# Optimization experiments

Measured on AMD Instinct MI355X. Metric: run time of the kernel, lower is better.

The kernel has to match this reference:

```python
import jax, jax.numpy as jnp
import numpy as np

IN_F, HID, OUT = 128, 128, 32
N_NODES, N_EDGES, N_GRAPHS = 100000, 1600000, 64


def gcn_conv(x, W, b, src, dst, n):
    """PyG-style GCNConv: add self-loops, symmetric deg^-1/2 norm, linear, scatter-add."""
    h = x @ W  # [N, F_out]
    loop = jnp.arange(n)
    src_f = jnp.concatenate([src, loop])
    dst_f = jnp.concatenate([dst, loop])
    deg = jax.ops.segment_sum(jnp.ones_like(dst_f, dtype=x.dtype), dst_f, num_segments=n)
    dinv = jax.lax.rsqrt(jnp.maximum(deg, 1.0))  # deg >= 1 because of self-loops
    norm = dinv[src_f] * dinv[dst_f]             # [E+N]
    msg = h[src_f] * norm[:, None]               # gather + scale, [E+N, F_out]
    out = jax.ops.segment_sum(msg, dst_f, num_segments=n)  # scatter-add
    return out + b


def setup_inputs() -> dict:
    key = jax.random.key(0)
    ks = jax.random.split(key, 10)
    x = jax.random.normal(ks[0], (N_NODES, IN_F), dtype=jnp.float32)
    edge_index = jax.random.randint(ks[1], (2, N_EDGES), 0, N_NODES, dtype=jnp.int64)
    batch = jnp.sort(jax.random.randint(ks[2], (N_NODES,), 0, N_GRAPHS, dtype=jnp.int64))

    def glorot(k, fi, fo):
        s = np.sqrt(6.0 / (fi + fo)).astype(np.float32)
        return jax.random.uniform(k, (fi, fo), dtype=jnp.float32, minval=-s, maxval=s)

    return {
        "x": x,
        "edge_index": edge_index,
        "batch": batch,
        "num_graphs": N_GRAPHS,
        "W1": glorot(ks[3], IN_F, HID), "b1": jnp.zeros((HID,), jnp.float32),
        "W2": glorot(ks[4], HID, HID), "b2": jnp.zeros((HID,), jnp.float32),
        "W3": glorot(ks[5], HID, OUT), "b3": jnp.zeros((OUT,), jnp.float32),
    }


def reference(x, edge_index, batch, num_graphs, W1, b1, W2, b2, W3, b3):
    n = x.shape[0]
    src, dst = edge_index[0], edge_index[1]
    # Dropout is identity in eval mode.
    h = jax.nn.relu(gcn_conv(x, W1, b1, src, dst, n))
    h = jax.nn.relu(gcn_conv(h, W2, b2, src, dst, n))
    h = gcn_conv(h, W3, b3, src, dst, n)  # [N, OUT]
    # global_mean_pool over batch ids
    sums = jax.ops.segment_sum(h, batch, num_segments=num_graphs)
    cnts = jax.ops.segment_sum(jnp.ones((n,), h.dtype), batch, num_segments=num_graphs)
    x_global = sums / jnp.maximum(cnts, 1.0)[:, None]
    return h, x_global
```

## Files before the change

kernel.cpp:

```cpp
#include <hip/hip_runtime.h>
#include <hip/hip_bf16.h>


typedef unsigned int uint32;
typedef short short8 __attribute__((ext_vector_type(8)));
typedef float f32x4 __attribute__((ext_vector_type(4)));

#define BSH 7
#define MAXB 1024
#define BCH 8192

static __device__ __forceinline__ unsigned short f2bf(float f) {
    uint32 u = __float_as_uint(f);
    return (unsigned short)((u + 0x7fffu + ((u >> 16) & 1u)) >> 16);
}
static __device__ __forceinline__ float bf2f_lo(uint32 u) {
    return __uint_as_float(u << 16);
}
static __device__ __forceinline__ float bf2f_hi(uint32 u) {
    return __uint_as_float(u & 0xffff0000u);
}

__global__ __launch_bounds__(256) void zcnt_k(int* bcnt) {
    bcnt[blockIdx.x * 256 + threadIdx.x] = 0;
}

__global__ __launch_bounds__(256) void bhist_k(const int* __restrict__ dst, int E,
                                               int* __restrict__ bcnt) {
    __shared__ int h[MAXB];
    for (int i = threadIdx.x; i < MAXB; i += 256) h[i] = 0;
    __syncthreads();
    const int base = blockIdx.x * BCH;
    const int end = min(E, base + BCH);
    for (int e = base + (int)threadIdx.x; e < end; e += 256)
        atomicAdd(&h[__builtin_nontemporal_load(&dst[e]) >> BSH], 1);
    __syncthreads();
    for (int i = threadIdx.x; i < MAXB; i += 256)
        if (h[i]) atomicAdd(&bcnt[i], h[i]);
}

__global__ __launch_bounds__(256) void bscan_k(const int* __restrict__ bcnt,
                                               int* __restrict__ bstart,
                                               int* __restrict__ bcur, int B) {
    __shared__ int tot[256];
    const int tid = threadIdx.x;
    int v[4];
    int s = 0;
#pragma unroll
    for (int j = 0; j < 4; j++) {
        int idx = tid * 4 + j;
        v[j] = (idx < B) ? bcnt[idx] : 0;
        s += v[j];
    }
    tot[tid] = s;
    __syncthreads();
    for (int o = 1; o < 256; o <<= 1) {
        int t = (tid >= o) ? tot[tid - o] : 0;
        __syncthreads();
        tot[tid] += t;
        __syncthreads();
    }
    int run = tot[tid] - s;
#pragma unroll
    for (int j = 0; j < 4; j++) {
        int idx = tid * 4 + j;
        if (idx < B) {
            bstart[idx] = run;
            bcur[idx] = run;
            run += v[j];
        }
    }
    if (tid == 255) bstart[B] = run;
}

__global__ __launch_bounds__(256) void bfill_k(const int* __restrict__ src,
                                               const int* __restrict__ dst, int E,
                                               int* __restrict__ bcur,
                                               int* __restrict__ fifo) {
    __shared__ int h[MAXB];
    __shared__ int base[MAXB];
    for (int i = threadIdx.x; i < MAXB; i += 256) h[i] = 0;
    __syncthreads();
    const int b0 = blockIdx.x * BCH;
    const int end = min(E, b0 + BCH);
    for (int e = b0 + (int)threadIdx.x; e < end; e += 256)
        atomicAdd(&h[__builtin_nontemporal_load(&dst[e]) >> BSH], 1);
    __syncthreads();
    for (int i = threadIdx.x; i < MAXB; i += 256) {
        int c = h[i];
        base[i] = c ? atomicAdd(&bcur[i], c) : 0;
        h[i] = 0;
    }
    __syncthreads();
    for (int e = b0 + (int)threadIdx.x; e < end; e += 256) {
        int d = __builtin_nontemporal_load(&dst[e]);
        int s = __builtin_nontemporal_load(&src[e]);
        int b = d >> BSH;
        int off = base[b] + atomicAdd(&h[b], 1);
        fifo[off] = s | ((d & 127) << 20);
    }
}

__global__ __launch_bounds__(256) void bdeg_k(const int* __restrict__ fifo,
                                              const int* __restrict__ bstart,
                                              int* __restrict__ deg, int M) {
    __shared__ int h[128];
    const int t = threadIdx.x;
    if (t < 128) h[t] = 0;
    __syncthreads();
    const int lo = bstart[blockIdx.x], hi = bstart[blockIdx.x + 1];
    for (int i = lo + t; i < hi; i += 256)
        atomicAdd(&h[fifo[i] >> 20], 1);
    __syncthreads();
    int node = (blockIdx.x << BSH) + t;
    if (t < 128 && node < M) deg[node] = 1 + h[t];
}

__global__ __launch_bounds__(256) void mkdinv_k(const int* __restrict__ deg,
                                                float* __restrict__ dinv, int M) {
    int i = blockIdx.x * 256 + threadIdx.x;
    if (i < M) dinv[i] = rsqrtf((float)deg[i]);
}

__global__ __launch_bounds__(256) void scan1_k(const int* __restrict__ deg, int M,
                                               int* __restrict__ blksum) {
    __shared__ int sh[256];
    int i = blockIdx.x * 256 + threadIdx.x;
    int v = (i < M) ? deg[i] - 1 : 0;
    sh[threadIdx.x] = v;
    __syncthreads();
    for (int o = 128; o > 0; o >>= 1) {
        if (threadIdx.x < o) sh[threadIdx.x] += sh[threadIdx.x + o];
        __syncthreads();
    }
    if (threadIdx.x == 0) blksum[blockIdx.x] = sh[0];
}

__global__ __launch_bounds__(512) void scan2_k(int* __restrict__ blksum, int nb) {
    __shared__ int sh[512];
    int tid = threadIdx.x;
    int v = (tid < nb) ? blksum[tid] : 0;
    sh[tid] = v;
    __syncthreads();
    for (int o = 1; o < 512; o <<= 1) {
        int t = (tid >= o) ? sh[tid - o] : 0;
        __syncthreads();
        sh[tid] += t;
        __syncthreads();
    }
    if (tid < nb) blksum[tid] = sh[tid] - v;
}

__global__ __launch_bounds__(256) void scan3_k(const int* __restrict__ deg, int M,
                                               const int* __restrict__ blksum,
                                               int* __restrict__ rowptr,
                                               int* __restrict__ cursor) {
    __shared__ int sh[256];
    int tid = threadIdx.x;
    int i = blockIdx.x * 256 + tid;
    int v = (i < M) ? deg[i] - 1 : 0;
    sh[tid] = v;
    __syncthreads();
    for (int o = 1; o < 256; o <<= 1) {
        int t = (tid >= o) ? sh[tid - o] : 0;
        __syncthreads();
        sh[tid] += t;
        __syncthreads();
    }
    int excl = sh[tid] - v + blksum[blockIdx.x];
    if (i < M) {
        rowptr[i] = excl;
        cursor[i] = excl;
    }
    if (i == M - 1) rowptr[M] = excl + v;
}

__global__ __launch_bounds__(256) void bcol_k(const int* __restrict__ fifo,
                                              const int* __restrict__ bstart,
                                              int* __restrict__ cursor,
                                              int* __restrict__ col) {
    const int lo = bstart[blockIdx.x], hi = bstart[blockIdx.x + 1];
    const int nbase = blockIdx.x << BSH;
    for (int i = lo + (int)threadIdx.x; i < hi; i += 256) {
        int ev = fifo[i];
        int node = nbase + (ev >> 20);
        int slot = atomicAdd(&cursor[node], 1);
        col[slot] = ev & 0xFFFFF;
    }
}

__global__ __launch_bounds__(256) void cvt_k(const float* __restrict__ x,
                                             unsigned short* __restrict__ o,
                                             int n8) {
    int i = blockIdx.x * 256 + threadIdx.x;
    if (i >= n8) return;
    const float4* xp = (const float4*)x + (size_t)i * 2;
    float4 a = xp[0], b = xp[1];
    union { unsigned short us[8]; uint4 v; } u;
    u.us[0] = f2bf(a.x); u.us[1] = f2bf(a.y); u.us[2] = f2bf(a.z); u.us[3] = f2bf(a.w);
    u.us[4] = f2bf(b.x); u.us[5] = f2bf(b.y); u.us[6] = f2bf(b.z); u.us[7] = f2bf(b.w);
    *((uint4*)o + i) = u.v;
}

__global__ __launch_bounds__(256) void wt_k(const float* __restrict__ W,
                                            unsigned short* __restrict__ Wt,
                                            int N) {
    int idx = blockIdx.x * 256 + threadIdx.x;
    if (idx >= N * 128) return;
    int n = idx >> 7, k = idx & 127;
    Wt[idx] = f2bf(W[k * N + n]);
}

template <int NT>
__global__ __launch_bounds__(256) void mgemm_k(const unsigned short* __restrict__ A,
                                               const unsigned short* __restrict__ Wt,
                                               const float* __restrict__ dinv,
                                               unsigned short* __restrict__ C,
                                               int M, int nstrips) {
    constexpr int N = NT * 16;
    const int lane = threadIdx.x & 63;
    const int wid = threadIdx.x >> 6;
    const int r = lane & 15;
    const int g = lane >> 4;

    short8 wf[NT][4];
#pragma unroll
    for (int t = 0; t < NT; t++)
#pragma unroll
        for (int s = 0; s < 4; s++)
            wf[t][s] = *(const short8*)&Wt[(size_t)(t * 16 + r) * 128 + s * 32 + g * 8];

    const int stride = gridDim.x * 4;
    for (int strip = blockIdx.x * 4 + wid; strip < nstrips; strip += stride) {
        const int R = strip * 16;
        const int ar = min(R + r, M - 1);
        short8 af[4];
#pragma unroll
        for (int s = 0; s < 4; s++)
            af[s] = *(const short8*)&A[(size_t)ar * 128 + s * 32 + g * 8];
        f32x4 acc[NT];
#pragma unroll
        for (int t = 0; t < NT; t++) acc[t] = (f32x4){0.f, 0.f, 0.f, 0.f};
#pragma unroll
        for (int s = 0; s < 4; s++)
#pragma unroll
            for (int t = 0; t < NT; t++)
                acc[t] = __builtin_amdgcn_mfma_f32_16x16x32_bf16(
                    af[s], wf[t][s], acc[t], 0, 0, 0);
#pragma unroll
        for (int j = 0; j < 4; j++) {
            int row = R + 4 * g + j;
            if (row < M) {
                float dv = dinv[row];
#pragma unroll
                for (int t = 0; t < NT; t++)
                    C[(size_t)row * N + t * 16 + r] = f2bf(dv * acc[t][j]);
            }
        }
    }
}

__global__ __launch_bounds__(256) void agg128_k(const unsigned short* __restrict__ Hb,
                                                const int* __restrict__ rowptr,
                                                const int* __restrict__ col,
                                                const float* __restrict__ dinv,
                                                const float* __restrict__ bias,
                                                unsigned short* __restrict__ outb,
                                                int M, int relu) {
    int node = blockIdx.x * 4 + (threadIdx.x >> 6);
    if (node >= M) return;
    int lane = threadIdx.x & 63;
    const uint32* Hu = (const uint32*)Hb;
    uint32 su = Hu[(size_t)node * 64 + lane];
    float ax = bf2f_lo(su);
    float ay = bf2f_hi(su);
    const int s = rowptr[node], e = rowptr[node + 1];

    for (int base = s; base < e; base += 64) {
        int n = e - base;
        if (n > 64) n = 64;
        int cid = __builtin_nontemporal_load(&col[base + (lane < n ? lane : 0)]);
        int j = 0;
        for (; j + 8 <= n; j += 8) {
            int sj[8]; uint32 u[8];
#pragma unroll
            for (int k = 0; k < 8; k++) sj[k] = __shfl(cid, j + k);
#pragma unroll
            for (int k = 0; k < 8; k++) u[k] = Hu[(size_t)sj[k] * 64 + lane];
#pragma unroll
            for (int k = 0; k < 8; k++) {
                ax += bf2f_lo(u[k]);
                ay += bf2f_hi(u[k]);
            }
        }
        for (; j < n; j++) {
            int s0 = __shfl(cid, j);
            uint32 u0 = Hu[(size_t)s0 * 64 + lane];
            ax += bf2f_lo(u0);
            ay += bf2f_hi(u0);
        }
    }
    float dv = dinv[node];
    float2 bv = *(const float2*)&bias[lane * 2];
    float ox = fmaf(dv, ax, bv.x), oy = fmaf(dv, ay, bv.y);
    if (relu) { ox = fmaxf(ox, 0.f); oy = fmaxf(oy, 0.f); }
    uint32 pk = (uint32)f2bf(ox) | ((uint32)f2bf(oy) << 16);
    *(uint32*)&outb[(size_t)node * 128 + lane * 2] = pk;
}

__global__ __launch_bounds__(256) void agg32_k(const unsigned short* __restrict__ Hb,
                                               const int* __restrict__ rowptr,
                                               const int* __restrict__ col,
                                               const float* __restrict__ dinv,
                                               const float* __restrict__ bias,
                                               float* __restrict__ out, int M) {
    int node = blockIdx.x * 4 + (threadIdx.x >> 6);
    if (node >= M) return;
    int lane = threadIdx.x & 63;
    int f = lane & 31;
    int half = lane >> 5;
    float acc = 0.f;
    if (!half)
        acc = __uint_as_float(((uint32)Hb[(size_t)node * 32 + f]) << 16);
    const int s = rowptr[node], e = rowptr[node + 1];
    int i = s + half;
    for (; i + 6 < e; i += 8) {
        int s0 = __builtin_nontemporal_load(&col[i]);
        int s1 = __builtin_nontemporal_load(&col[i + 2]);
        int s2 = __builtin_nontemporal_load(&col[i + 4]);
        int s3 = __builtin_nontemporal_load(&col[i + 6]);
        float h0 = __uint_as_float(((uint32)Hb[(size_t)s0 * 32 + f]) << 16);
        float h1 = __uint_as_float(((uint32)Hb[(size_t)s1 * 32 + f]) << 16);
        float h2 = __uint_as_float(((uint32)Hb[(size_t)s2 * 32 + f]) << 16);
        float h3 = __uint_as_float(((uint32)Hb[(size_t)s3 * 32 + f]) << 16);
        acc += h0 + h1 + h2 + h3;
    }
    for (; i < e; i += 2) {
        int s0 = __builtin_nontemporal_load(&col[i]);
        acc += __uint_as_float(((uint32)Hb[(size_t)s0 * 32 + f]) << 16);
    }
    acc += __shfl_xor(acc, 32);
    if (!half) out[(size_t)node * 32 + f] = fmaf(dinv[node], acc, bias[f]);
}

__global__ __launch_bounds__(256) void pool_k(const float* __restrict__ h,
                                              const int* __restrict__ batch, int M,
                                              float* __restrict__ out) {
    int g = blockIdx.x;
    int lo, hi;
    {
        int l = 0, r = M;
        while (l < r) { int m = (l + r) >> 1; if (batch[m] < g) l = m + 1; else r = m; }
        lo = l;
    }
    {
        int l = lo, r = M;
        while (l < r) { int m = (l + r) >> 1; if (batch[m] < g + 1) l = m + 1; else r = m; }
        hi = l;
    }
    int f = threadIdx.x & 31;
    int chunk = threadIdx.x >> 5;
    float acc = 0.f;
    for (int i = lo + chunk; i < hi; i += 8) acc += h[(size_t)i * 32 + f];
    __shared__ float red[8][32];
    red[chunk][f] = acc;
    __syncthreads();
    if (threadIdx.x < 32) {
        float s = 0.f;
#pragma unroll
        for (int c = 0; c < 8; c++) s += red[c][f];
        out[g * 32 + f] = s / fmaxf((float)(hi - lo), 1.f);
    }
}

extern "C" void kernel_launch(void* const* d_in, const int* in_sizes, int n_in,
                              void* d_out, int out_size, void* d_ws, size_t ws_size,
                              hipStream_t stream) {
    const float* x   = (const float*)d_in[0];
    const int* ei    = (const int*)d_in[1];
    const int* batch = (const int*)d_in[2];
    const float* W1  = (const float*)d_in[4];
    const float* b1  = (const float*)d_in[5];
    const float* W2  = (const float*)d_in[6];
    const float* b2  = (const float*)d_in[7];
    const float* W3  = (const float*)d_in[8];
    const float* b3  = (const float*)d_in[9];

    const int M = in_sizes[0] / 128;
    const int E = in_sizes[1] / 2;
    const int G = 64;
    const int* srcp = ei;
    const int* dstp = ei + E;
    const int B = (M + 127) >> BSH;

    char* p = (char*)d_ws;
    auto carve = [&](size_t bytes) {
        void* r = (void*)p;
        p += (bytes + 255) & ~(size_t)255;
        return r;
    };
    int*   deg    = (int*)carve((size_t)M * 4);
    float* dinv   = (float*)carve((size_t)M * 4);
    int*   rowptr = (int*)carve((size_t)(M + 1) * 4);
    int*   cursor = (int*)carve((size_t)M * 4);
    int*   blksum = (int*)carve(512 * 4);
    int*   bcnt   = (int*)carve(MAXB * 4);
    int*   bstart = (int*)carve((MAXB + 1) * 4);
    int*   bcur   = (int*)carve(MAXB * 4);
    int*   fifo   = (int*)carve((size_t)E * 4);
    int*   col    = (int*)carve((size_t)E * 4);
    unsigned short* Xb  = (unsigned short*)carve((size_t)M * 128 * 2);
    unsigned short* Hb  = (unsigned short*)carve((size_t)M * 128 * 2);
    unsigned short* Ob  = (unsigned short*)carve((size_t)M * 128 * 2);
    unsigned short* H3  = (unsigned short*)carve((size_t)M * 32 * 2);
    unsigned short* Wt1 = (unsigned short*)carve(128 * 128 * 2);
    unsigned short* Wt2 = (unsigned short*)carve(128 * 128 * 2);
    unsigned short* Wt3 = (unsigned short*)carve(32 * 128 * 2);

    float* outh = (float*)d_out;
    float* outg = outh + (size_t)M * 32;

    const int nbM = (M + 255) / 256;
    const int nbE = (E + BCH - 1) / BCH;
    const int nstrips = (M + 15) / 16;
    const int gblk = (nstrips + 7) / 8;

    cvt_k<<<(M * 128 / 8 + 255) / 256, 256, 0, stream>>>(x, Xb, M * 128 / 8);
    zcnt_k<<<MAXB / 256, 256, 0, stream>>>(bcnt);
    bhist_k<<<nbE, 256, 0, stream>>>(dstp, E, bcnt);
    bscan_k<<<1, 256, 0, stream>>>(bcnt, bstart, bcur, B);
    bfill_k<<<nbE, 256, 0, stream>>>(srcp, dstp, E, bcur, fifo);
    bdeg_k<<<B, 256, 0, stream>>>(fifo, bstart, deg, M);
    mkdinv_k<<<nbM, 256, 0, stream>>>(deg, dinv, M);
    scan1_k<<<nbM, 256, 0, stream>>>(deg, M, blksum);
    scan2_k<<<1, 512, 0, stream>>>(blksum, nbM);
    scan3_k<<<nbM, 256, 0, stream>>>(deg, M, blksum, rowptr, cursor);
    bcol_k<<<B, 256, 0, stream>>>(fifo, bstart, cursor, col);
    wt_k<<<(128 * 128 + 255) / 256, 256, 0, stream>>>(W1, Wt1, 128);
    wt_k<<<(128 * 128 + 255) / 256, 256, 0, stream>>>(W2, Wt2, 128);
    wt_k<<<(32 * 128 + 255) / 256, 256, 0, stream>>>(W3, Wt3, 32);

    mgemm_k<8><<<gblk, 256, 0, stream>>>(Xb, Wt1, dinv, Hb, M, nstrips);
    agg128_k<<<(M + 3) / 4, 256, 0, stream>>>(Hb, rowptr, col, dinv, b1, Ob, M, 1);
    mgemm_k<8><<<gblk, 256, 0, stream>>>(Ob, Wt2, dinv, Hb, M, nstrips);
    agg128_k<<<(M + 3) / 4, 256, 0, stream>>>(Hb, rowptr, col, dinv, b2, Ob, M, 1);
    mgemm_k<2><<<gblk, 256, 0, stream>>>(Ob, Wt3, dinv, H3, M, nstrips);
    agg32_k<<<(M + 3) / 4, 256, 0, stream>>>(H3, rowptr, col, dinv, b3, outh, M);
    pool_k<<<G, 256, 0, stream>>>(outh, batch, M, outg);
}
```

Before: 536.4 us.

## Fuse fp32→bf16 conversion into GEMM, reuse block histograms, merge weight transposes, deepen gathers

The first GEMM now reads fp32 x directly and converts to bf16 in registers, which removes the separate conversion kernel and its intermediate buffer round-trip. bhist_k writes per-block histograms so bfill_k no longer rescans dst to rebuild them. The three weight-transpose launches become one kernel. The 128-wide and 32-wide aggregation loops get deeper unrolling (16 and 8 gathers in flight) to expose more memory-level parallelism. In exchange, the first GEMM moves twice the input bytes, the new histogram buffer costs extra workspace and writes, and register pressure rises.

```diff
diff --git a/kernel.cpp b/kernel.cpp
--- a/kernel.cpp
+++ b/kernel.cpp
@@ -26,7 +26,8 @@
 }
 
 __global__ __launch_bounds__(256) void bhist_k(const int* __restrict__ dst, int E,
-                                               int* __restrict__ bcnt) {
+                                               int* __restrict__ bcnt,
+                                               int* __restrict__ blkhist) {
     __shared__ int h[MAXB];
     for (int i = threadIdx.x; i < MAXB; i += 256) h[i] = 0;
     __syncthreads();
@@ -35,8 +36,12 @@
     for (int e = base + (int)threadIdx.x; e < end; e += 256)
         atomicAdd(&h[__builtin_nontemporal_load(&dst[e]) >> BSH], 1);
     __syncthreads();
-    for (int i = threadIdx.x; i < MAXB; i += 256)
-        if (h[i]) atomicAdd(&bcnt[i], h[i]);
+    int* bh = blkhist + (size_t)blockIdx.x * MAXB;
+    for (int i = threadIdx.x; i < MAXB; i += 256) {
+        int c = h[i];
+        __builtin_nontemporal_store(c, &bh[i]);
+        if (c) atomicAdd(&bcnt[i], c);
+    }
 }
 
 __global__ __launch_bounds__(256) void bscan_k(const int* __restrict__ bcnt,
@@ -75,23 +80,20 @@
 
 __global__ __launch_bounds__(256) void bfill_k(const int* __restrict__ src,
                                                const int* __restrict__ dst, int E,
+                                               const int* __restrict__ blkhist,
                                                int* __restrict__ bcur,
                                                int* __restrict__ fifo) {
     __shared__ int h[MAXB];
     __shared__ int base[MAXB];
-    for (int i = threadIdx.x; i < MAXB; i += 256) h[i] = 0;
+    const int* bh = blkhist + (size_t)blockIdx.x * MAXB;
+    for (int i = threadIdx.x; i < MAXB; i += 256) {
+        int c = bh[i];
+        base[i] = c ? atomicAdd(&bcur[i], c) : 0;
+        h[i] = 0;
+    }
     __syncthreads();
     const int b0 = blockIdx.x * BCH;
     const int end = min(E, b0 + BCH);
-    for (int e = b0 + (int)threadIdx.x; e < end; e += 256)
-        atomicAdd(&h[__builtin_nontemporal_load(&dst[e]) >> BSH], 1);
-    __syncthreads();
-    for (int i = threadIdx.x; i < MAXB; i += 256) {
-        int c = h[i];
-        base[i] = c ? atomicAdd(&bcur[i], c) : 0;
-        h[i] = 0;
-    }
-    __syncthreads();
     for (int e = b0 + (int)threadIdx.x; e < end; e += 256) {
         int d = __builtin_nontemporal_load(&dst[e]);
         int s = __builtin_nontemporal_load(&src[e]);
@@ -189,30 +191,22 @@
     }
 }
 
-__global__ __launch_bounds__(256) void cvt_k(const float* __restrict__ x,
-                                             unsigned short* __restrict__ o,
-                                             int n8) {
-    int i = blockIdx.x * 256 + threadIdx.x;
-    if (i >= n8) return;
-    const float4* xp = (const float4*)x + (size_t)i * 2;
-    float4 a = xp[0], b = xp[1];
-    union { unsigned short us[8]; uint4 v; } u;
-    u.us[0] = f2bf(a.x); u.us[1] = f2bf(a.y); u.us[2] = f2bf(a.z); u.us[3] = f2bf(a.w);
-    u.us[4] = f2bf(b.x); u.us[5] = f2bf(b.y); u.us[6] = f2bf(b.z); u.us[7] = f2bf(b.w);
-    *((uint4*)o + i) = u.v;
-}
-
-__global__ __launch_bounds__(256) void wt_k(const float* __restrict__ W,
-                                            unsigned short* __restrict__ Wt,
-                                            int N) {
+__global__ __launch_bounds__(256) void wtall_k(const float* __restrict__ W1,
+                                               const float* __restrict__ W2,
+                                               const float* __restrict__ W3,
+                                               unsigned short* __restrict__ Wtall) {
     int idx = blockIdx.x * 256 + threadIdx.x;
-    if (idx >= N * 128) return;
-    int n = idx >> 7, k = idx & 127;
-    Wt[idx] = f2bf(W[k * N + n]);
-}
-
-template <int NT>
-__global__ __launch_bounds__(256) void mgemm_k(const unsigned short* __restrict__ A,
+    if (idx >= 288 * 128) return;
+    int r = idx >> 7, k = idx & 127;
+    float v;
+    if (r < 128)      v = W1[k * 128 + r];
+    else if (r < 256) v = W2[k * 128 + (r - 128)];
+    else              v = W3[k * 32 + (r - 256)];
+    Wtall[idx] = f2bf(v);
+}
+
+template <int NT, bool F32A>
+__global__ __launch_bounds__(256) void mgemm_k(const void* __restrict__ Av,
                                                const unsigned short* __restrict__ Wt,
                                                const float* __restrict__ dinv,
                                                unsigned short* __restrict__ C,
@@ -236,8 +230,22 @@
         const int ar = min(R + r, M - 1);
         short8 af[4];
 #pragma unroll
-        for (int s = 0; s < 4; s++)
-            af[s] = *(const short8*)&A[(size_t)ar * 128 + s * 32 + g * 8];
+        for (int s = 0; s < 4; s++) {
+            if (F32A) {
+                const float* A = (const float*)Av;
+                float4 a0 = *(const float4*)&A[(size_t)ar * 128 + s * 32 + g * 8];
+                float4 a1 = *(const float4*)&A[(size_t)ar * 128 + s * 32 + g * 8 + 4];
+                short8 v;
+                v[0] = (short)f2bf(a0.x); v[1] = (short)f2bf(a0.y);
+                v[2] = (short)f2bf(a0.z); v[3] = (short)f2bf(a0.w);
+                v[4] = (short)f2bf(a1.x); v[5] = (short)f2bf(a1.y);
+                v[6] = (short)f2bf(a1.z); v[7] = (short)f2bf(a1.w);
+                af[s] = v;
+            } else {
+                const unsigned short* A = (const unsigned short*)Av;
+                af[s] = *(const short8*)&A[(size_t)ar * 128 + s * 32 + g * 8];
+            }
+        }
         f32x4 acc[NT];
 #pragma unroll
         for (int t = 0; t < NT; t++) acc[t] = (f32x4){0.f, 0.f, 0.f, 0.f};
@@ -281,6 +289,18 @@
         if (n > 64) n = 64;
         int cid = __builtin_nontemporal_load(&col[base + (lane < n ? lane : 0)]);
         int j = 0;
+        for (; j + 16 <= n; j += 16) {
+            int sj[16]; uint32 u[16];
+#pragma unroll
+            for (int k = 0; k < 16; k++) sj[k] = __shfl(cid, j + k);
+#pragma unroll
+            for (int k = 0; k < 16; k++) u[k] = Hu[(size_t)sj[k] * 64 + lane];
+#pragma unroll
+            for (int k = 0; k < 16; k++) {
+                ax += bf2f_lo(u[k]);
+                ay += bf2f_hi(u[k]);
+            }
+        }
         for (; j + 8 <= n; j += 8) {
             int sj[8]; uint32 u[8];
 #pragma unroll
@@ -324,16 +344,17 @@
         acc = __uint_as_float(((uint32)Hb[(size_t)node * 32 + f]) << 16);
     const int s = rowptr[node], e = rowptr[node + 1];
     int i = s + half;
-    for (; i + 6 < e; i += 8) {
-        int s0 = __builtin_nontemporal_load(&col[i]);
-        int s1 = __builtin_nontemporal_load(&col[i + 2]);
-        int s2 = __builtin_nontemporal_load(&col[i + 4]);
-        int s3 = __builtin_nontemporal_load(&col[i + 6]);
-        float h0 = __uint_as_float(((uint32)Hb[(size_t)s0 * 32 + f]) << 16);
-        float h1 = __uint_as_float(((uint32)Hb[(size_t)s1 * 32 + f]) << 16);
-        float h2 = __uint_as_float(((uint32)Hb[(size_t)s2 * 32 + f]) << 16);
-        float h3 = __uint_as_float(((uint32)Hb[(size_t)s3 * 32 + f]) << 16);
-        acc += h0 + h1 + h2 + h3;
+    for (; i + 14 < e; i += 16) {
+        int sj[8];
+#pragma unroll
+        for (int k = 0; k < 8; k++)
+            sj[k] = __builtin_nontemporal_load(&col[i + 2 * k]);
+        float hv[8];
+#pragma unroll
+        for (int k = 0; k < 8; k++)
+            hv[k] = __uint_as_float(((uint32)Hb[(size_t)sj[k] * 32 + f]) << 16);
+#pragma unroll
+        for (int k = 0; k < 8; k++) acc += hv[k];
     }
     for (; i < e; i += 2) {
         int s0 = __builtin_nontemporal_load(&col[i]);
@@ -392,6 +413,7 @@
     const int* srcp = ei;
     const int* dstp = ei + E;
     const int B = (M + 127) >> BSH;
+    const int nbE = (E + BCH - 1) / BCH;
 
     char* p = (char*)d_ws;
     auto carve = [&](size_t bytes) {
@@ -399,52 +421,49 @@
         p += (bytes + 255) & ~(size_t)255;
         return r;
     };
-    int*   deg    = (int*)carve((size_t)M * 4);
-    float* dinv   = (float*)carve((size_t)M * 4);
-    int*   rowptr = (int*)carve((size_t)(M + 1) * 4);
-    int*   cursor = (int*)carve((size_t)M * 4);
-    int*   blksum = (int*)carve(512 * 4);
-    int*   bcnt   = (int*)carve(MAXB * 4);
-    int*   bstart = (int*)carve((MAXB + 1) * 4);
-    int*   bcur   = (int*)carve(MAXB * 4);
-    int*   fifo   = (int*)carve((size_t)E * 4);
-    int*   col    = (int*)carve((size_t)E * 4);
-    unsigned short* Xb  = (unsigned short*)carve((size_t)M * 128 * 2);
-    unsigned short* Hb  = (unsigned short*)carve((size_t)M * 128 * 2);
-    unsigned short* Ob  = (unsigned short*)carve((size_t)M * 128 * 2);
-    unsigned short* H3  = (unsigned short*)carve((size_t)M * 32 * 2);
-    unsigned short* Wt1 = (unsigned short*)carve(128 * 128 * 2);
-    unsigned short* Wt2 = (unsigned short*)carve(128 * 128 * 2);
-    unsigned short* Wt3 = (unsigned short*)carve(32 * 128 * 2);
+    int*   deg     = (int*)carve((size_t)M * 4);
+    float* dinv    = (float*)carve((size_t)M * 4);
+    int*   rowptr  = (int*)carve((size_t)(M + 1) * 4);
+    int*   cursor  = (int*)carve((size_t)M * 4);
+    int*   blksum  = (int*)carve(512 * 4);
+    int*   bcnt    = (int*)carve(MAXB * 4);
+    int*   bstart  = (int*)carve((MAXB + 1) * 4);
+    int*   bcur    = (int*)carve(MAXB * 4);
+    int*   blkhist = (int*)carve((size_t)nbE * MAXB * 4);
+    int*   fifo    = (int*)carve((size_t)E * 4);
+    int*   col     = (int*)carve((size_t)E * 4);
+    unsigned short* Hb    = (unsigned short*)carve((size_t)M * 128 * 2);
+    unsigned short* Ob    = (unsigned short*)carve((size_t)M * 128 * 2);
+    unsigned short* H3    = (unsigned short*)carve((size_t)M * 32 * 2);
+    unsigned short* Wtall = (unsigned short*)carve(288 * 128 * 2);
+    unsigned short* Wt1 = Wtall;
+    unsigned short* Wt2 = Wtall + 128 * 128;
+    unsigned short* Wt3 = Wtall + 256 * 128;
 
     float* outh = (float*)d_out;
     float* outg = outh + (size_t)M * 32;
 
     const int nbM = (M + 255) / 256;
-    const int nbE = (E + BCH - 1) / BCH;
     const int nstrips = (M + 15) / 16;
     const int gblk = (nstrips + 7) / 8;
 
-    cvt_k<<<(M * 128 / 8 + 255) / 256, 256, 0, stream>>>(x, Xb, M * 128 / 8);
     zcnt_k<<<MAXB / 256, 256, 0, stream>>>(bcnt);
-    bhist_k<<<nbE, 256, 0, stream>>>(dstp, E, bcnt);
+    bhist_k<<<nbE, 256, 0, stream>>>(dstp, E, bcnt, blkhist);
     bscan_k<<<1, 256, 0, stream>>>(bcnt, bstart, bcur, B);
-    bfill_k<<<nbE, 256, 0, stream>>>(srcp, dstp, E, bcur, fifo);
+    bfill_k<<<nbE, 256, 0, stream>>>(srcp, dstp, E, blkhist, bcur, fifo);
     bdeg_k<<<B, 256, 0, stream>>>(fifo, bstart, deg, M);
     mkdinv_k<<<nbM, 256, 0, stream>>>(deg, dinv, M);
     scan1_k<<<nbM, 256, 0, stream>>>(deg, M, blksum);
     scan2_k<<<1, 512, 0, stream>>>(blksum, nbM);
     scan3_k<<<nbM, 256, 0, stream>>>(deg, M, blksum, rowptr, cursor);
     bcol_k<<<B, 256, 0, stream>>>(fifo, bstart, cursor, col);
-    wt_k<<<(128 * 128 + 255) / 256, 256, 0, stream>>>(W1, Wt1, 128);
-    wt_k<<<(128 * 128 + 255) / 256, 256, 0, stream>>>(W2, Wt2, 128);
-    wt_k<<<(32 * 128 + 255) / 256, 256, 0, stream>>>(W3, Wt3, 32);
-
-    mgemm_k<8><<<gblk, 256, 0, stream>>>(Xb, Wt1, dinv, Hb, M, nstrips);
+    wtall_k<<<(288 * 128 + 255) / 256, 256, 0, stream>>>(W1, W2, W3, Wtall);
+
+    mgemm_k<8, true><<<gblk, 256, 0, stream>>>(x, Wt1, dinv, Hb, M, nstrips);
     agg128_k<<<(M + 3) / 4, 256, 0, stream>>>(Hb, rowptr, col, dinv, b1, Ob, M, 1);
-    mgemm_k<8><<<gblk, 256, 0, stream>>>(Ob, Wt2, dinv, Hb, M, nstrips);
+    mgemm_k<8, false><<<gblk, 256, 0, stream>>>(Ob, Wt2, dinv, Hb, M, nstrips);
     agg128_k<<<(M + 3) / 4, 256, 0, stream>>>(Hb, rowptr, col, dinv, b2, Ob, M, 1);
-    mgemm_k<2><<<gblk, 256, 0, stream>>>(Ob, Wt3, dinv, H3, M, nstrips);
+    mgemm_k<2, false><<<gblk, 256, 0, stream>>>(Ob, Wt3, dinv, H3, M, nstrips);
     agg32_k<<<(M + 3) / 4, 256, 0, stream>>>(H3, rowptr, col, dinv, b3, outh, M);
     pool_k<<<G, 256, 0, stream>>>(outh, batch, M, outg);
 }
```

Result: no change. 543.8 us (+1.4%).
